# Kernel tuning notes

Hardware: AMD Instinct MI355X
Metric: run time of the kernel (lower is better)

The kernel has to match this reference:

```python
import jax, jax.numpy as jnp
import numpy as np
import math

D_MODEL = 1024
NUM_HEADS = 16
HEAD_DIM = D_MODEL // NUM_HEADS
EPS = 1e-6
ROPE_BASE = 10000.0


def _rope_cos_sin(seq_len, dim, dtype):
    inv_freq = 1.0 / (ROPE_BASE ** (jnp.arange(0, dim, 2, dtype=jnp.float32) / dim))
    t = jnp.arange(seq_len, dtype=jnp.float32)
    freqs = jnp.outer(t, inv_freq)                 # [s, dim/2]
    emb = jnp.concatenate([freqs, freqs], axis=-1)  # [s, dim]
    return jnp.cos(emb).astype(dtype), jnp.sin(emb).astype(dtype)


def _rotate_half(x):
    x1, x2 = jnp.split(x, 2, axis=-1)
    return jnp.concatenate([-x2, x1], axis=-1)


def setup_inputs() -> dict:
    key = jax.random.key(0)
    k1, k2, k3 = jax.random.split(key, 3)
    b, s = 2, 2048
    x = jax.random.normal(k1, (b, s, D_MODEL), dtype=jnp.float32)
    norm_w = jnp.ones((D_MODEL,), dtype=jnp.float32)
    qkv_w = jax.random.normal(k2, (3 * D_MODEL, D_MODEL), dtype=jnp.float32) * (1.0 / math.sqrt(D_MODEL))
    qkv_b = jnp.zeros((3 * D_MODEL,), dtype=jnp.float32)
    proj_w = jax.random.normal(k3, (D_MODEL, D_MODEL), dtype=jnp.float32) * (1.0 / math.sqrt(D_MODEL))
    proj_b = jnp.zeros((D_MODEL,), dtype=jnp.float32)
    return {"x": x, "norm_w": norm_w, "qkv_w": qkv_w, "qkv_b": qkv_b,
            "proj_w": proj_w, "proj_b": proj_b}


def reference(x, norm_w, qkv_w, qkv_b, proj_w, proj_b):
    b, s, d = x.shape
    # RMSNorm (pre-LN)
    xn = x * jax.lax.rsqrt(jnp.mean(x * x, axis=-1, keepdims=True) + EPS) * norm_w
    # Fused QKV
    qkv = jnp.einsum('bsd,ed->bse', xn, qkv_w) + qkv_b
    q, k, v = jnp.split(qkv, 3, axis=-1)
    # [b, h, s, hd]
    def shape(t):
        return t.reshape(b, s, NUM_HEADS, HEAD_DIM).transpose(0, 2, 1, 3)
    q, k, v = shape(q), shape(k), shape(v)
    # RoPE on head_dim
    cos, sin = _rope_cos_sin(s, HEAD_DIM, x.dtype)  # [s, hd]
    q = q * cos + _rotate_half(q) * sin
    k = k * cos + _rotate_half(k) * sin
    # Naive causal attention
    scale = 1.0 / math.sqrt(HEAD_DIM)
    scores = jnp.einsum('bhqd,bhkd->bhqk', q, k) * scale
    causal = jnp.tril(jnp.ones((s, s), dtype=bool))
    scores = jnp.where(causal, scores, -jnp.inf)
    attn = jax.nn.softmax(scores, axis=-1)
    y = jnp.einsum('bhqk,bhkd->bhqd', attn, v)
    y = y.transpose(0, 2, 1, 3).reshape(b, s, d)
    return jnp.einsum('bsd,ed->bse', y, proj_w) + proj_b
```

## Files before the change

kernel.cpp:

```cpp
#include <hip/hip_runtime.h>
#include <cstdint>
#include <cstddef>

#define NB 2
#define NS 2048
#define ND 1024
#define NH 16
#define HD 64
#define ROWS 4096
#define E3 3072

using bf16 = __bf16;
typedef __attribute__((ext_vector_type(4))) __bf16 bf16x4;
typedef __attribute__((ext_vector_type(8))) __bf16 bf16x8;
typedef __attribute__((ext_vector_type(4))) float f32x4;

__device__ __forceinline__ f32x4 mfma16(bf16x8 a, bf16x8 b, f32x4 c) {
    return __builtin_amdgcn_mfma_f32_16x16x32_bf16(a, b, c, 0, 0, 0);
}

__device__ __forceinline__ void gll16(const bf16* src, bf16* lds) {
    __builtin_amdgcn_global_load_lds(
        (const __attribute__((address_space(1))) void*)src,
        (__attribute__((address_space(3))) void*)lds, 16, 0, 0);
}

__global__ __launch_bounds__(256) void prep(const float* __restrict__ qkv_w,
                                            const float* __restrict__ proj_w,
                                            const float* __restrict__ x,
                                            const float* __restrict__ norm_w,
                                            bf16* __restrict__ wq,
                                            bf16* __restrict__ xn,
                                            float4* __restrict__ tab) {
    __shared__ float wsum[4];
    int bid = blockIdx.x;
    int tid = threadIdx.x;
    if (bid < 4096) {
        const int n1 = E3 * ND;
        int i = (bid * 256 + tid) * 4;
        const float* src = (i < n1) ? (qkv_w + i) : (proj_w + (i - n1));
        float4 v = *(const float4*)src;
        bf16x4 o;
        o[0] = (bf16)v.x; o[1] = (bf16)v.y; o[2] = (bf16)v.z; o[3] = (bf16)v.w;
        *(bf16x4*)(wq + i) = o;
    } else if (bid < 8192) {
        int row = bid - 4096;
        const float* xr = x + (size_t)row * ND;
        float4 v = ((const float4*)xr)[tid];
        float ss = v.x*v.x + v.y*v.y + v.z*v.z + v.w*v.w;
        #pragma unroll
        for (int m = 32; m >= 1; m >>= 1) ss += __shfl_xor(ss, m);
        if ((tid & 63) == 0) wsum[tid >> 6] = ss;
        __syncthreads();
        float total = wsum[0] + wsum[1] + wsum[2] + wsum[3];
        float scale = rsqrtf(total * (1.0f / ND) + 1e-6f);
        float4 wv = ((const float4*)norm_w)[tid];
        bf16x4 o;
        o[0] = (bf16)(v.x * scale * wv.x);
        o[1] = (bf16)(v.y * scale * wv.y);
        o[2] = (bf16)(v.z * scale * wv.z);
        o[3] = (bf16)(v.w * scale * wv.w);
        ((bf16x4*)(xn + (size_t)row * ND))[tid] = o;
    } else {
        int idx = (bid - 8192) * 256 + tid;
        int s = idx >> 4, j = idx & 15;
        float f0 = powf(10000.0f, -(float)j * (1.0f / 32.0f));
        float f1 = powf(10000.0f, -(float)(j + 16) * (1.0f / 32.0f));
        float sn0, c0, sn1, c1;
        sincosf((float)s * f0, &sn0, &c0);
        sincosf((float)s * f1, &sn1, &c1);
        tab[idx] = make_float4(c0, sn0, c1, sn1);
    }
}

__global__ __launch_bounds__(256) void gemm_qkv_rope(const bf16* __restrict__ A,
                                                     const bf16* __restrict__ Bm,
                                                     const float* __restrict__ bias,
                                                     const float4* __restrict__ tab,
                                                     bf16* __restrict__ Qb,
                                                     bf16* __restrict__ Kb,
                                                     bf16* __restrict__ Vf) {
    const int K = ND;
    __shared__ bf16 smem[16384];
    const int tid = threadIdx.x;
    const int wave = tid >> 6, lane = tid & 63;
    const int quad = lane >> 4, l15 = lane & 15;
    const int row0 = blockIdx.x * 128, col0 = blockIdx.y * 128;
    const int wr = (wave >> 1) * 64, wc = (wave & 1) * 64;
    const int srow = lane >> 2;
    const int scol = (lane & 3) * 8;

    f32x4 acc[4][4] = {};

    auto stage = [&](int k0, int p) {
        bf16* Ad = smem + p * 4096;
        bf16* Bd = smem + 8192 + p * 4096;
        #pragma unroll
        for (int i = 0; i < 2; ++i) {
            int r = wave * 32 + i * 16;
            gll16(A + (size_t)(row0 + r + srow) * K + k0 + scol, Ad + r * 32);
            gll16(Bm + (size_t)(col0 + r + srow) * K + k0 + scol, Bd + r * 32);
        }
    };

    stage(0, 0);
    __syncthreads();
    for (int k0 = 0; k0 < K; k0 += 32) {
        const int p = (k0 >> 5) & 1;
        if (k0 + 32 < K) stage(k0 + 32, p ^ 1);
        const bf16* As = smem + p * 4096;
        const bf16* Bs = smem + 8192 + p * 4096;
        bf16x8 af[4], bff[4];
        #pragma unroll
        for (int t = 0; t < 4; ++t) {
            af[t]  = *(const bf16x8*)(As + (wr + t * 16 + l15) * 32 + quad * 8);
            bff[t] = *(const bf16x8*)(Bs + (wc + t * 16 + l15) * 32 + quad * 8);
        }
        #pragma unroll
        for (int mt = 0; mt < 4; ++mt)
            #pragma unroll
            for (int nt = 0; nt < 4; ++nt)
                acc[mt][nt] = mfma16(af[mt], bff[nt], acc[mt][nt]);
        __syncthreads();
    }

    float bb[4];
    #pragma unroll
    for (int nt = 0; nt < 4; ++nt) bb[nt] = bias[col0 + wc + nt * 16 + l15];

    const int region = col0 >> 10;
    if (region == 2) {
        const int cv = col0 - 2048 + wc;
        const int h = cv >> 6;
        const int b = row0 >> 11;
        const int sloc = row0 & (NS - 1);
        const int kg0 = (sloc + wr) >> 5;
        bf16* vh = Vf + (size_t)(b * NH + h) * 131072;
        #pragma unroll
        for (int Gw = 0; Gw < 2; ++Gw) {
            #pragma unroll
            for (int nt = 0; nt < 4; ++nt) {
                bf16x8 vf8;
                #pragma unroll
                for (int r = 0; r < 4; ++r) {
                    vf8[r]     = (bf16)(acc[2 * Gw][nt][r] + bb[nt]);
                    vf8[4 + r] = (bf16)(acc[2 * Gw + 1][nt][r] + bb[nt]);
                }
                *(bf16x8*)(vh + ((size_t)(kg0 + Gw) * 4 + nt) * 512 + lane * 8) = vf8;
            }
        }
    } else {
        const float scale = (region == 0) ? 0.125f : 1.0f;
        bf16* Ob = (region == 0) ? Qb : Kb;
        const int h = ((col0 + wc) & 1023) >> 6;
        bf16* ep = smem + wave * 2048;
        #pragma unroll
        for (int p = 0; p < 2; ++p) {
            #pragma unroll
            for (int mtl = 0; mtl < 2; ++mtl) {
                const int mt = p * 2 + mtl;
                #pragma unroll
                for (int r = 0; r < 4; ++r) {
                    int row = row0 + wr + mt * 16 + quad * 4 + r;
                    int s = row & (NS - 1);
                    float4 cs = tab[s * 16 + l15];
                    #pragma unroll
                    for (int nt = 0; nt < 4; ++nt) {
                        float v  = acc[mt][nt][r] + bb[nt];
                        float vp = acc[mt][nt ^ 2][r] + bb[nt ^ 2];
                        float cc = (nt & 1) ? cs.z : cs.x;
                        float ss = (nt & 1) ? cs.w : cs.y;
                        float res = (nt < 2) ? (v * cc - vp * ss) : (v * cc + vp * ss);
                        ep[(mtl * 16 + quad * 4 + r) * 64 + nt * 16 + l15] = (bf16)(res * scale);
                    }
                }
            }
            asm volatile("s_waitcnt lgkmcnt(0)" ::: "memory");
            const int rowp = row0 + wr + p * 32;
            const int b = rowp >> 11;
            const int s0p = rowp & (NS - 1);
            bf16* gbase = Ob + ((size_t)(b * NH + h) * NS + s0p + (lane >> 3)) * 64 + (lane & 7) * 8;
            const bf16* lbase = ep + (lane >> 3) * 64 + (lane & 7) * 8;
            #pragma unroll
            for (int i = 0; i < 4; ++i) {
                bf16x8 v8 = *(const bf16x8*)(lbase + i * 512);
                *(bf16x8*)(gbase + (size_t)i * 512) = v8;
            }
            asm volatile("s_waitcnt lgkmcnt(0)" ::: "memory");
        }
    }
}

__global__ __launch_bounds__(256) void gemm_proj(const bf16* __restrict__ A,
                                                 const bf16* __restrict__ Bm,
                                                 const float* __restrict__ bias,
                                                 float* __restrict__ C) {
    __shared__ bf16 smem[12288];
    const int tid = threadIdx.x;
    const int wave = tid >> 6, lane = tid & 63;
    const int quad = lane >> 4, l15 = lane & 15;
    const int row0 = blockIdx.x * 128, col0 = blockIdx.y * 64;
    const int wr = (wave >> 1) * 64, wc = (wave & 1) * 32;
    const int srow = lane >> 2;
    const int scol = (lane & 3) * 8;

    f32x4 acc[4][2] = {};

    auto stage = [&](int k0, int p) {
        bf16* Ad = smem + p * 4096;
        bf16* Bd = smem + 8192 + p * 2048;
        gll16(A + (size_t)(row0 + wave * 32 + srow) * ND + k0 + scol, Ad + (wave * 32) * 32);
        gll16(A + (size_t)(row0 + wave * 32 + 16 + srow) * ND + k0 + scol, Ad + (wave * 32 + 16) * 32);
        gll16(Bm + (size_t)(col0 + wave * 16 + srow) * ND + k0 + scol, Bd + (wave * 16) * 32);
    };

    stage(0, 0);
    __syncthreads();
    for (int k0 = 0; k0 < ND; k0 += 32) {
        const int p = (k0 >> 5) & 1;
        if (k0 + 32 < ND) stage(k0 + 32, p ^ 1);
        const bf16* As = smem + p * 4096;
        const bf16* Bs = smem + 8192 + p * 2048;
        bf16x8 af[4], bff[2];
        #pragma unroll
        for (int t = 0; t < 4; ++t)
            af[t] = *(const bf16x8*)(As + (wr + t * 16 + l15) * 32 + quad * 8);
        #pragma unroll
        for (int t = 0; t < 2; ++t)
            bff[t] = *(const bf16x8*)(Bs + (wc + t * 16 + l15) * 32 + quad * 8);
        #pragma unroll
        for (int mt = 0; mt < 4; ++mt)
            #pragma unroll
            for (int nt = 0; nt < 2; ++nt)
                acc[mt][nt] = mfma16(af[mt], bff[nt], acc[mt][nt]);
        __syncthreads();
    }

    #pragma unroll
    for (int nt = 0; nt < 2; ++nt) {
        int col = col0 + wc + nt * 16 + l15;
        float bv = bias[col];
        #pragma unroll
        for (int mt = 0; mt < 4; ++mt) {
            int row = row0 + wr + mt * 16 + quad * 4;
            #pragma unroll
            for (int r = 0; r < 4; ++r)
                C[(size_t)(row + r) * ND + col] = acc[mt][nt][r] + bv;
        }
    }
}

__global__ __launch_bounds__(256) __attribute__((amdgpu_waves_per_eu(2, 2)))
void attn(const bf16* __restrict__ Q,
          const bf16* __restrict__ K,
          const bf16* __restrict__ Vf,
          bf16* __restrict__ Y) {
    __shared__ bf16 Ksm[2][8192];
    __shared__ bf16 Vsm[2][8192];
    int bid = blockIdx.x;
    int g = bid >> 5;
    int bh = bid & 31;
    int qt = (g < 8) ? (15 - g) : (g - 8);
    int tid = threadIdx.x;
    int wave = tid >> 6, lane = tid & 63;
    int quad = lane >> 4, l15 = lane & 15;
    int q0 = qt * 128 + wave * 32;
    const bf16* Qh = Q + (size_t)bh * NS * 64;
    const bf16* Kh = K + (size_t)bh * NS * 64;
    const float NEG_INF = -__builtin_inff();

    const int krow = wave * 8 + (lane >> 3);
    const int ksx  = (lane & 7) ^ (krow & 7);
    const bf16* sK = Kh + (size_t)krow * 64 + ksx * 8;
    const bf16* sV = Vf + (size_t)bh * 131072 + wave * 2048 + lane * 8;

    const bf16* pk0 = &Ksm[0][l15 * 64 + ((quad) ^ (l15 & 7)) * 8];
    const bf16* pk1 = &Ksm[0][l15 * 64 + ((4 + quad) ^ (l15 & 7)) * 8];
    const bf16* pvf = &Vsm[0][lane * 8];

    bf16x8 bq[2][2];
    #pragma unroll
    for (int t = 0; t < 2; ++t)
        #pragma unroll
        for (int hh = 0; hh < 2; ++hh)
            bq[t][hh] = *(const bf16x8*)(Qh + (size_t)(q0 + t * 16 + l15) * 64 + hh * 32 + quad * 8);

    f32x4 o[2][4] = {};
    float lsum[2] = {0.f, 0.f};

    auto stage = [&](int c, int par) {
        const int kb = c * 128;
        bf16* dK = &Ksm[par][wave * 512];
        bf16* dV = &Vsm[par][wave * 2048];
        #pragma unroll
        for (int i = 0; i < 4; ++i)
            gll16(sK + (size_t)(kb + i * 32) * 64, dK + i * 2048);
        #pragma unroll
        for (int nt = 0; nt < 4; ++nt)
            gll16(sV + (size_t)(kb >> 5) * 2048 + nt * 512, dV + nt * 512);
    };

    auto compute = [&](int cc, int par) {
        const int kb = cc * 128;
        const int pb = par * 8192;
        bf16x8 ak[4][4], vf[4][4];
        #pragma unroll
        for (int ksub = 0; ksub < 4; ++ksub) {
            ak[ksub][0] = *(const bf16x8*)(pk0 + pb + ksub * 2048);
            ak[ksub][1] = *(const bf16x8*)(pk1 + pb + ksub * 2048);
            ak[ksub][2] = *(const bf16x8*)(pk0 + pb + ksub * 2048 + 1024);
            ak[ksub][3] = *(const bf16x8*)(pk1 + pb + ksub * 2048 + 1024);
            vf[ksub][0] = *(const bf16x8*)(pvf + pb + ksub * 2048);
            vf[ksub][1] = *(const bf16x8*)(pvf + pb + ksub * 2048 + 512);
            vf[ksub][2] = *(const bf16x8*)(pvf + pb + ksub * 2048 + 1024);
            vf[ksub][3] = *(const bf16x8*)(pvf + pb + ksub * 2048 + 1536);
        }
        #pragma unroll
        for (int ksub = 0; ksub < 4; ++ksub) {
            const int kbs = kb + ksub * 32;
            if (kbs <= q0) {
                const bool masked = (kbs == q0);
                #pragma unroll
                for (int t = 0; t < 2; ++t) {
                    f32x4 sh0 = {}, sh1 = {};
                    sh0 = mfma16(ak[ksub][0], bq[t][0], sh0);
                    sh0 = mfma16(ak[ksub][1], bq[t][1], sh0);
                    sh1 = mfma16(ak[ksub][2], bq[t][0], sh1);
                    sh1 = mfma16(ak[ksub][3], bq[t][1], sh1);
                    if (masked) {
                        int qy = q0 + t * 16 + l15;
                        #pragma unroll
                        for (int r = 0; r < 4; ++r) {
                            if (kbs + quad * 4 + r > qy)      sh0[r] = NEG_INF;
                            if (kbs + 16 + quad * 4 + r > qy) sh1[r] = NEG_INF;
                        }
                    }
                    bf16x8 pa;
                    float ls = 0.f;
                    #pragma unroll
                    for (int j = 0; j < 4; ++j) {
                        float p0 = __expf(sh0[j]);
                        float p1 = __expf(sh1[j]);
                        ls += p0 + p1;
                        pa[j] = (bf16)p0;
                        pa[4 + j] = (bf16)p1;
                    }
                    lsum[t] += ls;
                    o[t][0] = mfma16(pa, vf[ksub][0], o[t][0]);
                    o[t][1] = mfma16(pa, vf[ksub][1], o[t][1]);
                    o[t][2] = mfma16(pa, vf[ksub][2], o[t][2]);
                    o[t][3] = mfma16(pa, vf[ksub][3], o[t][3]);
                }
            }
        }
    };

    const int ncb = qt + 1;
    stage(0, 0);
    __syncthreads();
    for (int c = 0; c < ncb; ++c) {
        const int par = c & 1;
        if (c + 1 < ncb) stage(c + 1, par ^ 1);
        compute(c, par);
        __syncthreads();
    }

    int b = bh >> 4, h = bh & 15;
    bf16* ep = &Ksm[0][wave * 2048];
    #pragma unroll
    for (int t = 0; t < 2; ++t) {
        float red = lsum[t];
        red += __shfl_xor(red, 16);
        red += __shfl_xor(red, 32);
        #pragma unroll
        for (int r = 0; r < 4; ++r) {
            float il = 1.0f / __shfl(red, quad * 4 + r);
            #pragma unroll
            for (int nt = 0; nt < 4; ++nt)
                ep[(t * 16 + quad * 4 + r) * 64 + nt * 16 + l15] = (bf16)(o[t][nt][r] * il);
        }
    }
    asm volatile("s_waitcnt lgkmcnt(0)" ::: "memory");
    bf16* gbase = Y + ((size_t)(b * NS + q0 + (lane >> 3)) << 10) + h * 64 + (lane & 7) * 8;
    const bf16* lbase = ep + (lane >> 3) * 64 + (lane & 7) * 8;
    #pragma unroll
    for (int i = 0; i < 4; ++i) {
        bf16x8 v8 = *(const bf16x8*)(lbase + i * 512);
        *(bf16x8*)(gbase + ((size_t)i * 8 << 10)) = v8;
    }
}

extern "C" void kernel_launch(void* const* d_in, const int* in_sizes, int n_in,
                              void* d_out, int out_size, void* d_ws, size_t ws_size,
                              hipStream_t stream) {
    const float* x      = (const float*)d_in[0];
    const float* norm_w = (const float*)d_in[1];
    const float* qkv_w  = (const float*)d_in[2];
    const float* qkv_b  = (const float*)d_in[3];
    const float* proj_w = (const float*)d_in[4];
    const float* proj_b = (const float*)d_in[5];
    float* out = (float*)d_out;

    char* ws = (char*)d_ws;
    size_t off = 0;
    bf16* xn    = (bf16*)(ws + off); off += (size_t)ROWS * ND * 2;
    bf16* wq    = (bf16*)(ws + off); off += (size_t)E3 * ND * 2;
    bf16* wp    = (bf16*)(ws + off); off += (size_t)ND * ND * 2;
    bf16* Qb    = (bf16*)(ws + off); off += (size_t)NB * NH * NS * HD * 2;
    bf16* Kb    = (bf16*)(ws + off); off += (size_t)NB * NH * NS * HD * 2;
    bf16* Vfrag = (bf16*)(ws + off); off += (size_t)NB * NH * HD * NS * 2;
    bf16* Y     = (bf16*)(ws + off); off += (size_t)ROWS * ND * 2;
    float4* tab = (float4*)(ws + off); off += (size_t)NS * 16 * sizeof(float4);

    prep<<<8320, 256, 0, stream>>>(qkv_w, proj_w, x, norm_w, wq, xn, tab);
    gemm_qkv_rope<<<dim3(ROWS / 128, E3 / 128), 256, 0, stream>>>(xn, wq, qkv_b, tab, Qb, Kb, Vfrag);
    attn<<<NB * NH * (NS / 128), 256, 0, stream>>>(Qb, Kb, Vfrag, Y);
    gemm_proj<<<dim3(ROWS / 128, ND / 64), 256, 0, stream>>>(Y, wp, proj_b, out);
}
```

Before: 172.8 us.

## Split causal attention into balanced KV-chunk work units with atomic accumulation

Replaces the one-block-per-query-tile attention launch with 512 blocks that each take a contiguous, nearly equal run of (head, query tile, KV chunk) units, using the softmax without a running max so partial results can simply be added. Partial O and row sums are accumulated into fp32 global buffers with atomicAdd, and a new normalize kernel divides and converts to bf16. This aims to remove the load imbalance from the triangular causal workload. In exchange it adds two memsets, a large number of fp32 atomics on a 16MB buffer, and an extra kernel pass.

```diff
diff --git a/kernel.cpp b/kernel.cpp
--- a/kernel.cpp
+++ b/kernel.cpp
@@ -254,42 +254,55 @@
 void attn(const bf16* __restrict__ Q,
           const bf16* __restrict__ K,
           const bf16* __restrict__ Vf,
-          bf16* __restrict__ Y) {
+          float* __restrict__ Yacc,
+          float* __restrict__ Lacc) {
     __shared__ bf16 Ksm[2][8192];
     __shared__ bf16 Vsm[2][8192];
-    int bid = blockIdx.x;
-    int g = bid >> 5;
-    int bh = bid & 31;
-    int qt = (g < 8) ? (15 - g) : (g - 8);
-    int tid = threadIdx.x;
-    int wave = tid >> 6, lane = tid & 63;
-    int quad = lane >> 4, l15 = lane & 15;
-    int q0 = qt * 128 + wave * 32;
-    const bf16* Qh = Q + (size_t)bh * NS * 64;
-    const bf16* Kh = K + (size_t)bh * NS * 64;
-    const float NEG_INF = -__builtin_inff();
+    const int blk = blockIdx.x;
+    const int len = 8 + (blk < 256 ? 1 : 0);
+    const int u0 = blk * 8 + (blk < 256 ? blk : 256);
+    const int tid = threadIdx.x;
+    const int wave = tid >> 6, lane = tid & 63;
+    const int quad = lane >> 4, l15 = lane & 15;
+
+    int bh = u0 / 136;
+    int rem = u0 - bh * 136;
+    int qt = 0;
+    while ((qt + 1) * (qt + 2) / 2 <= rem) ++qt;
+    int c = rem - qt * (qt + 1) / 2;
 
     const int krow = wave * 8 + (lane >> 3);
     const int ksx  = (lane & 7) ^ (krow & 7);
-    const bf16* sK = Kh + (size_t)krow * 64 + ksx * 8;
-    const bf16* sV = Vf + (size_t)bh * 131072 + wave * 2048 + lane * 8;
 
     const bf16* pk0 = &Ksm[0][l15 * 64 + ((quad) ^ (l15 & 7)) * 8];
     const bf16* pk1 = &Ksm[0][l15 * 64 + ((4 + quad) ^ (l15 & 7)) * 8];
     const bf16* pvf = &Vsm[0][lane * 8];
 
     bf16x8 bq[2][2];
-    #pragma unroll
-    for (int t = 0; t < 2; ++t)
-        #pragma unroll
-        for (int hh = 0; hh < 2; ++hh)
-            bq[t][hh] = *(const bf16x8*)(Qh + (size_t)(q0 + t * 16 + l15) * 64 + hh * 32 + quad * 8);
-
-    f32x4 o[2][4] = {};
-    float lsum[2] = {0.f, 0.f};
-
-    auto stage = [&](int c, int par) {
-        const int kb = c * 128;
+    f32x4 o[2][4];
+    float lsum[2];
+    int q0w = 0;
+
+    auto loadq = [&](int sbh, int sqt) {
+        const bf16* Qh = Q + (size_t)sbh * NS * 64;
+        q0w = sqt * 128 + wave * 32;
+        #pragma unroll
+        for (int t = 0; t < 2; ++t)
+            #pragma unroll
+            for (int hh = 0; hh < 2; ++hh)
+                bq[t][hh] = *(const bf16x8*)(Qh + (size_t)(q0w + t * 16 + l15) * 64 + hh * 32 + quad * 8);
+        #pragma unroll
+        for (int t = 0; t < 2; ++t) {
+            lsum[t] = 0.f;
+            #pragma unroll
+            for (int nt = 0; nt < 4; ++nt) o[t][nt] = f32x4{};
+        }
+    };
+
+    auto stage = [&](int sbh, int sc, int par) {
+        const int kb = sc * 128;
+        const bf16* sK = K + (size_t)sbh * NS * 64 + (size_t)krow * 64 + ksx * 8;
+        const bf16* sV = Vf + (size_t)sbh * 131072 + wave * 2048 + lane * 8;
         bf16* dK = &Ksm[par][wave * 512];
         bf16* dV = &Vsm[par][wave * 2048];
         #pragma unroll
@@ -301,7 +314,6 @@
     };
 
     auto compute = [&](int cc, int par) {
-        const int kb = cc * 128;
         const int pb = par * 8192;
         bf16x8 ak[4][4], vf[4][4];
         #pragma unroll
@@ -317,9 +329,9 @@
         }
         #pragma unroll
         for (int ksub = 0; ksub < 4; ++ksub) {
-            const int kbs = kb + ksub * 32;
-            if (kbs <= q0) {
-                const bool masked = (kbs == q0);
+            const int kbs = cc * 128 + ksub * 32;
+            if (kbs <= q0w) {
+                const bool masked = (kbs == q0w);
                 #pragma unroll
                 for (int t = 0; t < 2; ++t) {
                     f32x4 sh0 = {}, sh1 = {};
@@ -328,11 +340,11 @@
                     sh1 = mfma16(ak[ksub][2], bq[t][0], sh1);
                     sh1 = mfma16(ak[ksub][3], bq[t][1], sh1);
                     if (masked) {
-                        int qy = q0 + t * 16 + l15;
+                        int qy = q0w + t * 16 + l15;
                         #pragma unroll
                         for (int r = 0; r < 4; ++r) {
-                            if (kbs + quad * 4 + r > qy)      sh0[r] = NEG_INF;
-                            if (kbs + 16 + quad * 4 + r > qy) sh1[r] = NEG_INF;
+                            if (kbs + quad * 4 + r > qy)      sh0[r] = -__builtin_inff();
+                            if (kbs + 16 + quad * 4 + r > qy) sh1[r] = -__builtin_inff();
                         }
                     }
                     bf16x8 pa;
@@ -355,39 +367,61 @@
         }
     };
 
-    const int ncb = qt + 1;
-    stage(0, 0);
+    auto flush = [&](int fbh, int fqt) {
+        const int fb = fbh >> 4, fh = fbh & 15;
+        const int fq0 = fqt * 128 + wave * 32;
+        #pragma unroll
+        for (int t = 0; t < 2; ++t) {
+            float red = lsum[t];
+            red += __shfl_xor(red, 16);
+            red += __shfl_xor(red, 32);
+            if (quad == 0)
+                atomicAdd(Lacc + ((size_t)fbh * NS) + fq0 + t * 16 + l15, red);
+            #pragma unroll
+            for (int r = 0; r < 4; ++r) {
+                float* yrow = Yacc + (size_t)(fb * NS + fq0 + t * 16 + quad * 4 + r) * ND + fh * 64 + l15;
+                #pragma unroll
+                for (int nt = 0; nt < 4; ++nt)
+                    atomicAdd(yrow + nt * 16, o[t][nt][r]);
+            }
+        }
+    };
+
+    loadq(bh, qt);
+    stage(bh, c, 0);
     __syncthreads();
-    for (int c = 0; c < ncb; ++c) {
-        const int par = c & 1;
-        if (c + 1 < ncb) stage(c + 1, par ^ 1);
+    for (int i = 0; i < len; ++i) {
+        const int par = i & 1;
+        int bhn = bh, qtn = qt, cn = c + 1;
+        if (cn > qtn) { cn = 0; ++qtn; if (qtn > 15) { qtn = 0; ++bhn; } }
+        if (i + 1 < len) stage(bhn, cn, par ^ 1);
         compute(c, par);
         __syncthreads();
-    }
-
-    int b = bh >> 4, h = bh & 15;
-    bf16* ep = &Ksm[0][wave * 2048];
-    #pragma unroll
-    for (int t = 0; t < 2; ++t) {
-        float red = lsum[t];
-        red += __shfl_xor(red, 16);
-        red += __shfl_xor(red, 32);
-        #pragma unroll
-        for (int r = 0; r < 4; ++r) {
-            float il = 1.0f / __shfl(red, quad * 4 + r);
-            #pragma unroll
-            for (int nt = 0; nt < 4; ++nt)
-                ep[(t * 16 + quad * 4 + r) * 64 + nt * 16 + l15] = (bf16)(o[t][nt][r] * il);
-        }
-    }
-    asm volatile("s_waitcnt lgkmcnt(0)" ::: "memory");
-    bf16* gbase = Y + ((size_t)(b * NS + q0 + (lane >> 3)) << 10) + h * 64 + (lane & 7) * 8;
-    const bf16* lbase = ep + (lane >> 3) * 64 + (lane & 7) * 8;
-    #pragma unroll
-    for (int i = 0; i < 4; ++i) {
-        bf16x8 v8 = *(const bf16x8*)(lbase + i * 512);
-        *(bf16x8*)(gbase + ((size_t)i * 8 << 10)) = v8;
-    }
+        if (i + 1 < len) {
+            if (bhn != bh || qtn != qt) {
+                flush(bh, qt);
+                loadq(bhn, qtn);
+            }
+            bh = bhn; qt = qtn; c = cn;
+        }
+    }
+    flush(bh, qt);
+}
+
+__global__ __launch_bounds__(256) void normalize_y(const float* __restrict__ Yacc,
+                                                   const float* __restrict__ Lacc,
+                                                   bf16* __restrict__ Y) {
+    int i = (blockIdx.x * 256 + threadIdx.x) * 4;
+    int row = i >> 10;
+    int b = row >> 11;
+    int s = row & (NS - 1);
+    int h = (i >> 6) & 15;
+    float il = 1.0f / Lacc[((size_t)(b * NH + h)) * NS + s];
+    float4 v = *(const float4*)(Yacc + i);
+    bf16x4 oo;
+    oo[0] = (bf16)(v.x * il); oo[1] = (bf16)(v.y * il);
+    oo[2] = (bf16)(v.z * il); oo[3] = (bf16)(v.w * il);
+    *(bf16x4*)(Y + i) = oo;
 }
 
 extern "C" void kernel_launch(void* const* d_in, const int* in_sizes, int n_in,
@@ -411,9 +445,14 @@
     bf16* Vfrag = (bf16*)(ws + off); off += (size_t)NB * NH * HD * NS * 2;
     bf16* Y     = (bf16*)(ws + off); off += (size_t)ROWS * ND * 2;
     float4* tab = (float4*)(ws + off); off += (size_t)NS * 16 * sizeof(float4);
-
+    float* Yacc = (float*)(ws + off); off += (size_t)ROWS * ND * 4;
+    float* Lacc = (float*)(ws + off); off += (size_t)NB * NH * NS * 4;
+
+    hipMemsetAsync(Yacc, 0, (size_t)ROWS * ND * 4, stream);
+    hipMemsetAsync(Lacc, 0, (size_t)NB * NH * NS * 4, stream);
     prep<<<8320, 256, 0, stream>>>(qkv_w, proj_w, x, norm_w, wq, xn, tab);
     gemm_qkv_rope<<<dim3(ROWS / 128, E3 / 128), 256, 0, stream>>>(xn, wq, qkv_b, tab, Qb, Kb, Vfrag);
-    attn<<<NB * NH * (NS / 128), 256, 0, stream>>>(Qb, Kb, Vfrag, Y);
+    attn<<<512, 256, 0, stream>>>(Qb, Kb, Vfrag, Yacc, Lacc);
+    normalize_y<<<ROWS * ND / 1024, 256, 0, stream>>>(Yacc, Lacc, Y);
     gemm_proj<<<dim3(ROWS / 128, ND / 64), 256, 0, stream>>>(Y, wp, proj_b, out);
 }
```

New measurement: 191.6 us. +10.8%, slower.
